# Performance work log

Measured on AMD Instinct MI355X. Metric: run time of the kernel, lower is better.

Reference implementation:

```python
import jax, jax.numpy as jnp
import numpy as np

N_AC = 8192     # number of amacrine cells
N_BC = 8192     # number of bipolar-cell helpers
T_KERNEL = 52   # len(torch.arange(0.8, 0, -1/64)) with input_frequency=64


def setup_inputs() -> dict:
    key = jax.random.key(0)
    k_x, k_w, k_k, k_s, k_o = jax.random.split(key, 5)
    x = jax.random.normal(k_x, (N_BC, T_KERNEL), dtype=jnp.float32)
    bc_ac_weight = jax.random.normal(k_w, (N_AC, N_BC), dtype=jnp.float32) / np.sqrt(N_BC)
    ac_kernel = jax.random.normal(k_k, (N_AC, T_KERNEL), dtype=jnp.float32)
    # normalize kernel rows like compute_ac_kernel does
    ac_kernel = ac_kernel / jnp.linalg.norm(ac_kernel, axis=1, keepdims=True)
    # slopes come from exp(log_slope) in the original -> keep positive
    ac_sigmoid_slope = jax.random.uniform(k_s, (N_AC,), dtype=jnp.float32) + 0.5
    ac_sigmoid_offset = 0.1 * jax.random.normal(k_o, (N_AC,), dtype=jnp.float32)
    return {
        "x": x,
        "bc_ac_weight": bc_ac_weight,
        "ac_kernel": ac_kernel,
        "ac_sigmoid_slope": ac_sigmoid_slope,
        "ac_sigmoid_offset": ac_sigmoid_offset,
    }


def reference(x, bc_ac_weight, ac_kernel, ac_sigmoid_slope, ac_sigmoid_offset):
    """One AC feedback step.

    x:                (nBC, T)   BC activity history window
    bc_ac_weight:     (nAC, nBC) precomputed (exp of log weights)
    ac_kernel:        (nAC, T)   precomputed normalized double-exp kernel
    ac_sigmoid_slope: (nAC,)
    ac_sigmoid_offset:(nAC,)
    returns:          (nAC,)
    """
    t_kernel = ac_kernel.shape[-1]
    y = bc_ac_weight @ x  # (nAC, T)
    if y.shape[-1] < t_kernel:  # static-shape left zero-pad as in F.pad
        y = jnp.pad(y, ((0, 0), (t_kernel - y.shape[-1], 0)))
    s = jnp.sum(ac_kernel * y, axis=1)  # temporal weighted sum -> (nAC,)
    # precomputed_sigmoid: sigmoid with per-cell slope and offset
    return jax.nn.sigmoid(ac_sigmoid_slope * (s - ac_sigmoid_offset))
```

## Files before the change

kernel.cpp:

```cpp
#include <hip/hip_runtime.h>
#include <hip/hip_bf16.h>
#include <math.h>

#define N_AC  8192
#define N_BC  8192
#define T_K   52
#define T_PAD 64

#define KSPLIT 16
#define KSEG   (N_BC / KSPLIT)
#define RSTRIDE 72
#define TILE_BF16 (16 * RSTRIDE)

typedef __bf16 bf16x8 __attribute__((ext_vector_type(8)));
typedef __bf16 bf16x4 __attribute__((ext_vector_type(4)));
typedef float  f32x4  __attribute__((ext_vector_type(4)));

__global__ void xpose_kernel(const float* __restrict__ x, __bf16* __restrict__ xT) {
    int gt = blockIdx.x * blockDim.x + threadIdx.x;
    int b = gt & (N_BC - 1);
    int t = gt >> 13;
    float v = (t < T_K) ? x[b * T_K + t] : 0.0f;
    xT[gt] = (__bf16)v;
}

__global__ __launch_bounds__(256, 6) void ac_gemm_kernel(
    const float*  __restrict__ W,
    const __bf16* __restrict__ xT,
    const float*  __restrict__ kern,
    float*        __restrict__ partials)
{
    const int tid  = threadIdx.x;
    const int lane = tid & 63;
    const int wave = tid >> 6;
    const int quad = lane >> 4;
    const int l15  = lane & 15;
    const int a0   = blockIdx.x * 16;
    const int ksub = blockIdx.y * 4 + wave;
    const int kbeg = ksub * KSEG;

    __shared__ __bf16 As[4 * 2 * TILE_BF16];
    __bf16* tile0 = &As[wave * 2 * TILE_BF16];

    const int wr = lane >> 2;
    const int wc = lane & 3;
    const float* wbase = W + (size_t)(a0 + wr) * N_BC + wc * 4;

    f32x4 acc[4] = {};

    #pragma unroll 2
    for (int it = 0; it < KSEG / 64; ++it) {
        const int kb = kbeg + it * 64;
        __bf16* tile = tile0 + (it & 1) * TILE_BF16;

        #pragma unroll
        for (int j = 0; j < 4; ++j) {
            float4 f = *(const float4*)(wbase + kb + j * 16);
            bf16x4 h;
            h[0] = (__bf16)f.x; h[1] = (__bf16)f.y;
            h[2] = (__bf16)f.z; h[3] = (__bf16)f.w;
            *(bf16x4*)&tile[wr * RSTRIDE + j * 16 + wc * 4] = h;
        }

        #pragma unroll
        for (int s = 0; s < 2; ++s) {
            bf16x8 af = *(const bf16x8*)&tile[l15 * RSTRIDE + s * 32 + quad * 8];
            #pragma unroll
            for (int nt = 0; nt < 4; ++nt) {
                bf16x8 bf = *(const bf16x8*)(xT + (size_t)(nt * 16 + l15) * N_BC
                                             + kb + s * 32 + quad * 8);
                acc[nt] = __builtin_amdgcn_mfma_f32_16x16x32_bf16(af, bf, acc[nt], 0, 0, 0);
            }
        }
    }

    float p[4] = {0.f, 0.f, 0.f, 0.f};
    #pragma unroll
    for (int nt = 0; nt < 4; ++nt) {
        int t = nt * 16 + l15;
        if (t < T_K) {
            #pragma unroll
            for (int r = 0; r < 4; ++r) {
                int grow = a0 + quad * 4 + r;
                p[r] += acc[nt][r] * kern[grow * T_K + t];
            }
        }
    }
    #pragma unroll
    for (int m = 1; m <= 8; m <<= 1) {
        #pragma unroll
        for (int r = 0; r < 4; ++r) p[r] += __shfl_xor(p[r], m);
    }

    if (l15 == 0) {
        #pragma unroll
        for (int r = 0; r < 4; ++r)
            partials[ksub * N_AC + a0 + quad * 4 + r] = p[r];
    }
}

__global__ void ac_final_kernel(const float* __restrict__ partials,
                                const float* __restrict__ slope,
                                const float* __restrict__ offs,
                                float* __restrict__ out) {
    int a = blockIdx.x * blockDim.x + threadIdx.x;
    if (a >= N_AC) return;
    float s = 0.f;
    #pragma unroll
    for (int ks = 0; ks < KSPLIT; ++ks) s += partials[ks * N_AC + a];
    float z = slope[a] * (s - offs[a]);
    out[a] = 1.0f / (1.0f + __expf(-z));
}

extern "C" void kernel_launch(void* const* d_in, const int* in_sizes, int n_in,
                              void* d_out, int out_size, void* d_ws, size_t ws_size,
                              hipStream_t stream) {
    const float* x     = (const float*)d_in[0];
    const float* W     = (const float*)d_in[1];
    const float* kern  = (const float*)d_in[2];
    const float* slope = (const float*)d_in[3];
    const float* offs  = (const float*)d_in[4];
    float* out = (float*)d_out;

    __bf16* xT      = (__bf16*)d_ws;
    float* partials = (float*)((char*)d_ws + (size_t)T_PAD * N_BC * sizeof(__bf16));

    xpose_kernel<<<dim3(T_PAD * N_BC / 256), dim3(256), 0, stream>>>(x, xT);
    ac_gemm_kernel<<<dim3(N_AC / 16, KSPLIT / 4), dim3(256), 0, stream>>>(
        W, xT, kern, partials);
    ac_final_kernel<<<dim3(N_AC / 256), dim3(256), 0, stream>>>(
        partials, slope, offs, out);
}
```

Before: 414.9 us.

## Pre-pack x into MFMA fragment layout and prefetch W rows in register chunks

Replaces the bf16 transpose with a pack kernel that writes x directly in the per-lane MFMA B-fragment order, so the GEMM reads B with fully contiguous 16-byte loads per lane. Each wave now owns 16 distinct AC rows over the full K segment rather than a K sub-slice. It streams W in 256-wide chunks held in 16 float4 registers that are prefetched one chunk ahead while the current chunk is converted to LDS and consumed. The goal is better coalescing of W reads and more loads in flight to hide HBM latency on the 256MB fp32 W stream. The cost is higher register pressure, and launch bounds drop from 6 to 4 waves per SIMD.

```diff
diff --git a/kernel.cpp b/kernel.cpp
--- a/kernel.cpp
+++ b/kernel.cpp
@@ -9,24 +9,36 @@
 
 #define KSPLIT 16
 #define KSEG   (N_BC / KSPLIT)
-#define RSTRIDE 72
-#define TILE_BF16 (16 * RSTRIDE)
+#define CHUNK  256
+#define NCHUNK (KSEG / CHUNK)
+#define RSTRIDE 264
 
 typedef __bf16 bf16x8 __attribute__((ext_vector_type(8)));
 typedef __bf16 bf16x4 __attribute__((ext_vector_type(4)));
 typedef float  f32x4  __attribute__((ext_vector_type(4)));
 
-__global__ void xpose_kernel(const float* __restrict__ x, __bf16* __restrict__ xT) {
-    int gt = blockIdx.x * blockDim.x + threadIdx.x;
-    int b = gt & (N_BC - 1);
-    int t = gt >> 13;
-    float v = (t < T_K) ? x[b * T_K + t] : 0.0f;
-    xT[gt] = (__bf16)v;
+__global__ void bpack_kernel(const float* __restrict__ x, __bf16* __restrict__ Bp) {
+    int gid   = blockIdx.x * blockDim.x + threadIdx.x;
+    int lane  = gid & 63;
+    int group = gid >> 6;
+    int kblock = group >> 2;
+    int nt     = group & 3;
+    int quad = lane >> 4;
+    int l15  = lane & 15;
+    int t  = nt * 16 + l15;
+    int b0 = kblock * 32 + quad * 8;
+    bf16x8 v;
+    #pragma unroll
+    for (int j = 0; j < 8; ++j) {
+        float f = (t < T_K) ? x[(b0 + j) * T_K + t] : 0.0f;
+        v[j] = (__bf16)f;
+    }
+    *(bf16x8*)(Bp + (size_t)group * 512 + lane * 8) = v;
 }
 
-__global__ __launch_bounds__(256, 6) void ac_gemm_kernel(
+__global__ __launch_bounds__(256, 4) void ac_gemm_kernel(
     const float*  __restrict__ W,
-    const __bf16* __restrict__ xT,
+    const __bf16* __restrict__ Bp,
     const float*  __restrict__ kern,
     float*        __restrict__ partials)
 {
@@ -35,40 +47,46 @@
     const int wave = tid >> 6;
     const int quad = lane >> 4;
     const int l15  = lane & 15;
-    const int a0   = blockIdx.x * 16;
-    const int ksub = blockIdx.y * 4 + wave;
+    const int a0   = blockIdx.x * 64 + wave * 16;
+    const int ksub = blockIdx.y;
     const int kbeg = ksub * KSEG;
 
-    __shared__ __bf16 As[4 * 2 * TILE_BF16];
-    __bf16* tile0 = &As[wave * 2 * TILE_BF16];
+    __shared__ __bf16 As[4 * 16 * RSTRIDE];
+    __bf16* tile = &As[wave * 16 * RSTRIDE];
 
-    const int wr = lane >> 2;
-    const int wc = lane & 3;
-    const float* wbase = W + (size_t)(a0 + wr) * N_BC + wc * 4;
+    const float* wbase = W + (size_t)a0 * N_BC + lane * 4;
 
     f32x4 acc[4] = {};
 
-    #pragma unroll 2
-    for (int it = 0; it < KSEG / 64; ++it) {
-        const int kb = kbeg + it * 64;
-        __bf16* tile = tile0 + (it & 1) * TILE_BF16;
+    float4 pre[16];
+    #pragma unroll
+    for (int j = 0; j < 16; ++j)
+        pre[j] = *(const float4*)(wbase + (size_t)j * N_BC + kbeg);
+
+    for (int c = 0; c < NCHUNK; ++c) {
+        const int kc = kbeg + c * CHUNK;
 
         #pragma unroll
-        for (int j = 0; j < 4; ++j) {
-            float4 f = *(const float4*)(wbase + kb + j * 16);
+        for (int j = 0; j < 16; ++j) {
             bf16x4 h;
-            h[0] = (__bf16)f.x; h[1] = (__bf16)f.y;
-            h[2] = (__bf16)f.z; h[3] = (__bf16)f.w;
-            *(bf16x4*)&tile[wr * RSTRIDE + j * 16 + wc * 4] = h;
+            h[0] = (__bf16)pre[j].x; h[1] = (__bf16)pre[j].y;
+            h[2] = (__bf16)pre[j].z; h[3] = (__bf16)pre[j].w;
+            *(bf16x4*)&tile[j * RSTRIDE + lane * 4] = h;
+        }
+
+        if (c + 1 < NCHUNK) {
+            #pragma unroll
+            for (int j = 0; j < 16; ++j)
+                pre[j] = *(const float4*)(wbase + (size_t)j * N_BC + kc + CHUNK);
         }
 
         #pragma unroll
-        for (int s = 0; s < 2; ++s) {
+        for (int s = 0; s < 8; ++s) {
             bf16x8 af = *(const bf16x8*)&tile[l15 * RSTRIDE + s * 32 + quad * 8];
+            const size_t kblock = (size_t)(kc >> 5) + s;
             #pragma unroll
             for (int nt = 0; nt < 4; ++nt) {
-                bf16x8 bf = *(const bf16x8*)(xT + (size_t)(nt * 16 + l15) * N_BC
-                                             + kb + s * 32 + quad * 8);
+                bf16x8 bf = *(const bf16x8*)(Bp + (kblock * 4 + nt) * 512 + lane * 8);
                 acc[nt] = __builtin_amdgcn_mfma_f32_16x16x32_bf16(af, bf, acc[nt], 0, 0, 0);
             }
         }
@@ -122,12 +140,12 @@
     const float* offs  = (const float*)d_in[4];
     float* out = (float*)d_out;
 
-    __bf16* xT      = (__bf16*)d_ws;
-    float* partials = (float*)((char*)d_ws + (size_t)T_PAD * N_BC * sizeof(__bf16));
+    __bf16* Bp      = (__bf16*)d_ws;
+    float* partials = (float*)((char*)d_ws + (size_t)1024 * 512 * sizeof(__bf16));
 
-    xpose_kernel<<<dim3(T_PAD * N_BC / 256), dim3(256), 0, stream>>>(x, xT);
-    ac_gemm_kernel<<<dim3(N_AC / 16, KSPLIT / 4), dim3(256), 0, stream>>>(
-        W, xT, kern, partials);
+    bpack_kernel<<<dim3(65536 / 256), dim3(256), 0, stream>>>(x, Bp);
+    ac_gemm_kernel<<<dim3(N_AC / 64, KSPLIT), dim3(256), 0, stream>>>(
+        W, Bp, kern, partials);
     ac_final_kernel<<<dim3(N_AC / 256), dim3(256), 0, stream>>>(
         partials, slope, offs, out);
 }
```

After: 383.3 us. 7.6% less time.
